# Kernel optimization log

Measured on AMD Instinct MI355X. Metric: run time of the kernel, lower is better.

## Reference

```python
import jax, jax.numpy as jnp
import numpy as np

T, B, V = 512, 64, 1296
S = 30            # fixed target length per sample (targets are concatenated B*S)
BLANK = 0
NEG = -1e30       # -inf surrogate, safe under logaddexp


def setup_inputs() -> dict:
    key = jax.random.key(0)
    k1, k2, k3 = jax.random.split(key, 3)
    logits = jax.random.normal(k1, (T, B, V), dtype=jnp.float32)
    log_probs = jax.nn.log_softmax(logits, axis=-1)  # valid log-prob input to CTC
    # targets are gloss ids in [1, V) (blank=0 excluded), concatenated layout
    targets = jax.random.randint(k2, (B * S,), 1, V, dtype=jnp.int64)
    input_lengths = jax.random.randint(k3, (B,), T // 2, T + 1, dtype=jnp.int32)
    target_lengths = jnp.full((B,), S, dtype=jnp.int32)
    return {"log_probs": log_probs, "targets": targets,
            "input_lengths": input_lengths, "target_lengths": target_lengths}


def _ctc_loss(log_probs, targets2d, input_lengths, target_lengths):
    # log_probs: (T,B,V); targets2d: (B,S)
    L = 2 * S + 1
    b_idx = jnp.arange(B)
    # extended label sequence with interleaved blanks: (B, L)
    ext = jnp.zeros((B, L), dtype=targets2d.dtype).at[:, 1::2].set(targets2d)
    # emission log-probs on lattice positions: lp[t,b,l] = log_probs[t,b,ext[b,l]]
    lp = jnp.take_along_axis(log_probs,
                             jnp.broadcast_to(ext[None, :, :], (T, B, L)), axis=2)
    # skip transition allowed where ext[l] != blank and ext[l] != ext[l-2]
    ext_m2 = jnp.pad(ext[:, :-2], ((0, 0), (2, 0)), constant_values=BLANK)
    allow = (ext != BLANK) & (ext != ext_m2)  # (B, L)

    alpha0 = jnp.full((B, L), NEG, dtype=log_probs.dtype)
    alpha0 = alpha0.at[:, 0].set(lp[0, :, 0]).at[:, 1].set(lp[0, :, 1])

    def step(alpha, lp_t):
        prev1 = jnp.pad(alpha[:, :-1], ((0, 0), (1, 0)), constant_values=NEG)
        prev2 = jnp.pad(alpha[:, :-2], ((0, 0), (2, 0)), constant_values=NEG)
        m = jnp.logaddexp(alpha, prev1)
        m = jnp.where(allow, jnp.logaddexp(m, prev2), m)
        new = m + lp_t
        return new, new

    _, alphas = jax.lax.scan(step, alpha0, lp[1:])          # (T-1, B, L)
    alphas = jnp.concatenate([alpha0[None], alphas], axis=0)  # (T, B, L)

    # alpha at each sample's final frame
    alpha_T = alphas[input_lengths - 1, b_idx]               # (B, L)
    tl = target_lengths.astype(jnp.int32)
    a_last_blank = alpha_T[b_idx, 2 * tl]
    a_last_label = alpha_T[b_idx, 2 * tl - 1]
    loss = -jnp.logaddexp(a_last_blank, a_last_label)        # (B,)
    # zero_infinity=True: infeasible alignments contribute 0
    loss = jnp.where(loss >= 1e29, 0.0, loss)
    # reduction='mean': per-sample loss / target_length, then batch mean
    return jnp.mean(loss / target_lengths.astype(loss.dtype))


def reference(log_probs, targets, input_lengths, target_lengths):
    targets2d = targets.reshape(B, S)  # all target_lengths == S (concatenated layout)
    return _ctc_loss(log_probs, targets2d, input_lengths, target_lengths)
```

## Files before the change

### kernel.cpp

```cpp
#include <hip/hip_runtime.h>

#define T_DIM 512
#define B_DIM 64
#define V_DIM 1296
#define S_DIM 30
#define LN2   0.6931471805599453f

template<int CTRL, bool BC>
__device__ __forceinline__ float dppf(float src, float old) {
    return __int_as_float(__builtin_amdgcn_update_dpp(
        __float_as_int(old), __float_as_int(src), CTRL, 0xF, 0xF, BC));
}

struct ScanSt { float p0, p1; int E; };

template<int MODE>
__device__ __forceinline__ void consume_chunk(const float2* __restrict__ ringc,
                                              int c, int len, int jl, bool is16,
                                              float skipw, int l, ScanSt& st)
{
    float p0 = st.p0, p1 = st.p1;
    int   E  = st.E;
    float2 buf[8];
#pragma unroll
    for (int i = 0; i < 8; ++i) buf[i] = ringc[i * 32 + jl];
#pragma unroll
    for (int i = 0; i < 32; ++i) {
        float2 w = buf[i & 7];
        if (i + 8 < 32) buf[i & 7] = ringc[(i + 8) * 32 + jl];
        if (MODE == 0 && i == 0) {
            p0 = (l == 0) ? ldexpf(w.x, 64) : 0.f;
            p1 = (l == 0) ? ldexpf(w.y, 64) : 0.f;
            E = 64;
        } else {
            float shr = dppf<0x111, true >(p1, 0.f);
            float bcv = dppf<0x142, false>(p1, p1);
            float p1m = is16 ? bcv : shr;
            float np1 = fmaf(skipw, p1m, p0 + p1) * w.y;
            float np0 = (p0 + p1m) * w.x;
            if (MODE == 2) {
                bool act = (c * 32 + i) < len;
                p0 = act ? np0 : p0;
                p1 = act ? np1 : p1;
            } else {
                p0 = np0; p1 = np1;
            }
        }
        if ((i & 7) == 7) {
            float m = fmaxf(p0, p1);
            m = fmaxf(m, dppf<0x111, true >(m, 0.f));
            m = fmaxf(m, dppf<0x112, true >(m, 0.f));
            m = fmaxf(m, dppf<0x114, true >(m, 0.f));
            m = fmaxf(m, dppf<0x118, true >(m, 0.f));
            m = fmaxf(m, dppf<0x142, false>(m, m));
            int eb  = (__float_as_int(m) >> 23) & 0xFF;
            int e31 = __builtin_amdgcn_readlane(eb, 31);
            int s   = 191 - e31;
            p0 = ldexpf(p0, s);
            p1 = ldexpf(p1, s);
            E += s;
        }
    }
    st.p0 = p0; st.p1 = p1; st.E = E;
}

__device__ __forceinline__ void stage_chunk(int k, int b, int trow, int lab, int p,
                                            const float* __restrict__ lp,
                                            float2* __restrict__ ring)
{
    int t0 = k * 32 + trow;
    const float* r0 = lp + ((size_t)t0 * B_DIM + b) * V_DIM;
    const float* r1 = r0 + (size_t)16 * B_DIM * V_DIM;
    float b0 = r0[0], l0 = r0[lab];
    float b1 = r1[0], l1 = r1[lab];
    float2* slot = ring + (size_t)(k & 3) * 1024;
    slot[p]       = make_float2(__expf(b0), __expf(l0));
    slot[p + 512] = make_float2(__expf(b1), __expf(l1));
}

__global__ __launch_bounds__(576)
void ctc_fused_kernel(const float* __restrict__ log_probs,
                      const int*   __restrict__ targets,
                      const int*   __restrict__ input_lengths,
                      const int*   __restrict__ target_lengths,
                      float*       __restrict__ loss_ws)
{
    __shared__ float2 ring[4 * 1024];
    const int  b    = blockIdx.x;
    const int  tid  = threadIdx.x;
    const int  len  = input_lengths[b];
    const bool prod = (tid < 512);

    const int j    = tid & 31;
    const int trow = (tid & 511) >> 5;
    int lab = 0;
    const int l  = tid - 512;
    const int jl = tid & 31;
    ScanSt st = {0.f, 0.f, 0};
    float skipw = 0.f;
    bool  is16  = false;

    if (prod) {
        lab = (j < S_DIM) ? targets[b * S_DIM + j] : 0;
        stage_chunk(0, b, trow, lab, tid, log_probs, ring);
        stage_chunk(1, b, trow, lab, tid, log_probs, ring);
        stage_chunk(2, b, trow, lab, tid, log_probs, ring);
    } else {
        is16 = (l == 16);
        bool allow = (l == 0);
        if (l >= 1 && l < S_DIM)
            allow = (targets[b * S_DIM + l] != targets[b * S_DIM + l - 1]);
        skipw = allow ? 1.f : 0.f;
    }
    __syncthreads();

    for (int c = 0; c < 16; ++c) {
        if (prod) {
            if (c < 13) stage_chunk(c + 3, b, trow, lab, tid, log_probs, ring);
        } else {
            const float2* ringc = ring + (size_t)(c & 3) * 1024;
            if (c == 0)                   consume_chunk<0>(ringc, c, len, jl, is16, skipw, l, st);
            else if ((c + 1) * 32 <= len) consume_chunk<1>(ringc, c, len, jl, is16, skipw, l, st);
            else if (c * 32 < len)        consume_chunk<2>(ringc, c, len, jl, is16, skipw, l, st);
        }
        __syncthreads();
    }

    if (!prod) {
        float pB = __shfl(st.p0, 30);
        float pL = __shfl(st.p1, 29);
        if (l == 0) {
            int   tl   = target_lengths[b];
            float sum  = pB + pL;
            float loss = -LN2 * (__builtin_amdgcn_logf(sum) - (float)st.E);
            if (!(loss < 1e29f)) loss = 0.f;
            loss_ws[b] = loss / (float)tl;
        }
    }
}

__global__ __launch_bounds__(64)
void ctc_reduce_kernel(const float* __restrict__ loss_ws, float* __restrict__ out)
{
    float v = loss_ws[threadIdx.x];
#pragma unroll
    for (int off = 32; off >= 1; off >>= 1)
        v += __shfl_xor(v, off);
    if (threadIdx.x == 0) out[0] = v / (float)B_DIM;
}

extern "C" void kernel_launch(void* const* d_in, const int* in_sizes, int n_in,
                              void* d_out, int out_size, void* d_ws, size_t ws_size,
                              hipStream_t stream)
{
    const float* log_probs      = (const float*)d_in[0];
    const int*   targets        = (const int*)  d_in[1];
    const int*   input_lengths  = (const int*)  d_in[2];
    const int*   target_lengths = (const int*)  d_in[3];
    float*       out            = (float*)d_out;
    float*       losses         = (float*)d_ws;

    hipLaunchKernelGGL(ctc_fused_kernel, dim3(B_DIM), dim3(576), 0, stream,
                       log_probs, targets, input_lengths, target_lengths, losses);
    hipLaunchKernelGGL(ctc_reduce_kernel, dim3(1), dim3(64), 0, stream, losses, out);
}
```

Measured before the change: 32.37 us.

## Pack four lattice states per lane, prefetch rows into registers, fuse final reduction

The scan wave now holds four lattice states per lane as packed float2 vectors, so the 61-state lattice fits in 16 lanes and the max reduction needs fewer DPP steps. Those reduction steps are spread across iterations so they overlap with the recurrence. Producers prefetch log-prob rows into registers two chunks ahead and write float4 ring entries, which hides global latency behind the barriers. The separate reduce kernel is replaced by an atomic counter with a last-block reduction, which adds a memset and a global atomic in exchange for one fewer kernel launch.

```diff
diff --git a/kernel.cpp b/kernel.cpp
--- a/kernel.cpp
+++ b/kernel.cpp
@@ -6,76 +6,87 @@
 #define S_DIM 30
 #define LN2   0.6931471805599453f
 
+typedef float v2f __attribute__((ext_vector_type(2)));
+
 template<int CTRL, bool BC>
 __device__ __forceinline__ float dppf(float src, float old) {
     return __int_as_float(__builtin_amdgcn_update_dpp(
         __float_as_int(old), __float_as_int(src), CTRL, 0xF, 0xF, BC));
 }
 
-struct ScanSt { float p0, p1; int E; };
-
 template<int MODE>
-__device__ __forceinline__ void consume_chunk(const float2* __restrict__ ringc,
-                                              int c, int len, int jl, bool is16,
-                                              float skipw, int l, ScanSt& st)
-{
-    float p0 = st.p0, p1 = st.p1;
-    int   E  = st.E;
-    float2 buf[8];
+__device__ __forceinline__ void consume_chunk(const float4* __restrict__ ringc,
+                                              int c, int len, int lane, v2f S,
+                                              v2f& X, v2f& Y, int& E)
+{
+    const int jl = lane & 15;
+    float4 buf[8];
 #pragma unroll
-    for (int i = 0; i < 8; ++i) buf[i] = ringc[i * 32 + jl];
+    for (int i = 0; i < 8; ++i) buf[i] = ringc[i * 16 + jl];
+
+    float mred = 0.f;
 #pragma unroll
     for (int i = 0; i < 32; ++i) {
-        float2 w = buf[i & 7];
-        if (i + 8 < 32) buf[i & 7] = ringc[(i + 8) * 32 + jl];
+        float4 w = buf[i & 7];
+        if (i + 8 < 32) buf[i & 7] = ringc[(i + 8) * 16 + jl];
+
         if (MODE == 0 && i == 0) {
-            p0 = (l == 0) ? ldexpf(w.x, 64) : 0.f;
-            p1 = (l == 0) ? ldexpf(w.y, 64) : 0.f;
+            bool l0 = (lane == 0);
+            X = (v2f){ l0 ? ldexpf(w.z, 64) : 0.f, 0.f };
+            Y = (v2f){ l0 ? ldexpf(w.x, 64) : 0.f, 0.f };
             E = 64;
         } else {
-            float shr = dppf<0x111, true >(p1, 0.f);
-            float bcv = dppf<0x142, false>(p1, p1);
-            float p1m = is16 ? bcv : shr;
-            float np1 = fmaf(skipw, p1m, p0 + p1) * w.y;
-            float np0 = (p0 + p1m) * w.x;
+            float q3m = dppf<0x111, true>(Y.y, 0.f);
+            v2f Z  = { q3m, Y.x };
+            v2f T1 = X + Z;
+            v2f T2 = X + Y;
+            v2f T3 = __builtin_elementwise_fma(S, Z, T2);
+            v2f Wb = { w.z, w.w };
+            v2f Wl = { w.x, w.y };
+            v2f Xn = T1 * Wb;
+            v2f Yn = T3 * Wl;
             if (MODE == 2) {
                 bool act = (c * 32 + i) < len;
-                p0 = act ? np0 : p0;
-                p1 = act ? np1 : p1;
-            } else {
-                p0 = np0; p1 = np1;
-            }
-        }
+                X = act ? Xn : X;
+                Y = act ? Yn : Y;
+            } else { X = Xn; Y = Yn; }
+        }
+
+        if ((i & 7) == 3) mred = fmaxf(fmaxf(X.x, X.y), fmaxf(Y.x, Y.y));
+        if ((i & 7) == 4) mred = fmaxf(mred, dppf<0x111, true>(mred, 0.f));
+        if ((i & 7) == 5) mred = fmaxf(mred, dppf<0x112, true>(mred, 0.f));
+        if ((i & 7) == 6) mred = fmaxf(mred, dppf<0x114, true>(mred, 0.f));
         if ((i & 7) == 7) {
-            float m = fmaxf(p0, p1);
-            m = fmaxf(m, dppf<0x111, true >(m, 0.f));
-            m = fmaxf(m, dppf<0x112, true >(m, 0.f));
-            m = fmaxf(m, dppf<0x114, true >(m, 0.f));
-            m = fmaxf(m, dppf<0x118, true >(m, 0.f));
-            m = fmaxf(m, dppf<0x142, false>(m, m));
-            int eb  = (__float_as_int(m) >> 23) & 0xFF;
-            int e31 = __builtin_amdgcn_readlane(eb, 31);
-            int s   = 191 - e31;
-            p0 = ldexpf(p0, s);
-            p1 = ldexpf(p1, s);
+            mred = fmaxf(mred, dppf<0x118, true>(mred, 0.f));
+            int e15 = (__builtin_amdgcn_readlane(__float_as_int(mred), 15) >> 23) & 0xFF;
+            int s = 191 - e15;
+            X = (v2f){ ldexpf(X.x, s), ldexpf(X.y, s) };
+            Y = (v2f){ ldexpf(Y.x, s), ldexpf(Y.y, s) };
             E += s;
         }
     }
-    st.p0 = p0; st.p1 = p1; st.E = E;
-}
-
-__device__ __forceinline__ void stage_chunk(int k, int b, int trow, int lab, int p,
-                                            const float* __restrict__ lp,
-                                            float2* __restrict__ ring)
-{
-    int t0 = k * 32 + trow;
-    const float* r0 = lp + ((size_t)t0 * B_DIM + b) * V_DIM;
-    const float* r1 = r0 + (size_t)16 * B_DIM * V_DIM;
-    float b0 = r0[0], l0 = r0[lab];
-    float b1 = r1[0], l1 = r1[lab];
-    float2* slot = ring + (size_t)(k & 3) * 1024;
-    slot[p]       = make_float2(__expf(b0), __expf(l0));
-    slot[p + 512] = make_float2(__expf(b1), __expf(l1));
+}
+
+struct PReg { float a, b, c; };
+
+__device__ __forceinline__ PReg load_rows(const float* __restrict__ lpb,
+                                          int k, int r, int lab0, int lab1)
+{
+    const float* row = lpb + (size_t)(k * 32 + r) * (B_DIM * V_DIM);
+    PReg x;
+    x.a = row[lab0];
+    x.b = row[lab1];
+    x.c = row[0];
+    return x;
+}
+
+__device__ __forceinline__ void write_chunk(float4* __restrict__ ring, int k, int p,
+                                            int q, const PReg& x)
+{
+    float wz = __expf(x.c);
+    float wx = (q < 15) ? __expf(x.a) : 0.f;
+    float wy = (q < 15) ? __expf(x.b) : 0.f;
+    ring[(size_t)(k & 3) * 512 + p] = make_float4(wx, wy, wz, wz);
 }
 
 __global__ __launch_bounds__(576)
@@ -83,70 +94,91 @@
                       const int*   __restrict__ targets,
                       const int*   __restrict__ input_lengths,
                       const int*   __restrict__ target_lengths,
-                      float*       __restrict__ loss_ws)
-{
-    __shared__ float2 ring[4 * 1024];
+                      float*       __restrict__ losses,
+                      unsigned*    __restrict__ counter,
+                      float*       __restrict__ out)
+{
+    __shared__ float4 ring[4 * 512];
     const int  b    = blockIdx.x;
     const int  tid  = threadIdx.x;
     const int  len  = input_lengths[b];
     const bool prod = (tid < 512);
 
-    const int j    = tid & 31;
-    const int trow = (tid & 511) >> 5;
-    int lab = 0;
-    const int l  = tid - 512;
-    const int jl = tid & 31;
-    ScanSt st = {0.f, 0.f, 0};
-    float skipw = 0.f;
-    bool  is16  = false;
+    const int q = tid & 15;
+    const int r = (tid & 511) >> 4;
+    int lab0 = 0, lab1 = 0;
+    PReg rA = {0,0,0}, rB = {0,0,0};
+    const float* lpb = log_probs + (size_t)b * V_DIM;
+
+    const int lane = tid - 512;
+    v2f X = {0.f, 0.f}, Y = {0.f, 0.f}, S = {0.f, 0.f};
+    int E = 0;
 
     if (prod) {
-        lab = (j < S_DIM) ? targets[b * S_DIM + j] : 0;
-        stage_chunk(0, b, trow, lab, tid, log_probs, ring);
-        stage_chunk(1, b, trow, lab, tid, log_probs, ring);
-        stage_chunk(2, b, trow, lab, tid, log_probs, ring);
+        int i0 = b * S_DIM + ((2 * q     < S_DIM) ? 2 * q     : 0);
+        int i1 = b * S_DIM + ((2 * q + 1 < S_DIM) ? 2 * q + 1 : 0);
+        lab0 = targets[i0];
+        lab1 = targets[i1];
+        PReg t0 = load_rows(lpb, 0, r, lab0, lab1);
+        PReg t1 = load_rows(lpb, 1, r, lab0, lab1);
+        PReg t2 = load_rows(lpb, 2, r, lab0, lab1);
+        rA = load_rows(lpb, 3, r, lab0, lab1);
+        rB = load_rows(lpb, 4, r, lab0, lab1);
+        write_chunk(ring, 0, tid, q, t0);
+        write_chunk(ring, 1, tid, q, t1);
+        write_chunk(ring, 2, tid, q, t2);
     } else {
-        is16 = (l == 16);
-        bool allow = (l == 0);
-        if (l >= 1 && l < S_DIM)
-            allow = (targets[b * S_DIM + l] != targets[b * S_DIM + l - 1]);
-        skipw = allow ? 1.f : 0.f;
+        int lq = lane & 15;
+        float s0 = 0.f, s1 = 0.f;
+        if (lq < 15) {
+            int k0 = 2 * lq;
+            int tc = targets[b * S_DIM + k0];
+            int tp = (k0 > 0) ? targets[b * S_DIM + k0 - 1] : -1;
+            s0 = (tc != tp) ? 1.f : 0.f;
+            int tn = targets[b * S_DIM + k0 + 1];
+            s1 = (tn != tc) ? 1.f : 0.f;
+        }
+        S = (v2f){ s0, s1 };
     }
     __syncthreads();
 
     for (int c = 0; c < 16; ++c) {
         if (prod) {
-            if (c < 13) stage_chunk(c + 3, b, trow, lab, tid, log_probs, ring);
+            if (c < 13) write_chunk(ring, c + 3, tid, q, rA);
+            PReg nl = {0,0,0};
+            if (c < 11) nl = load_rows(lpb, c + 5, r, lab0, lab1);
+            rA = rB; rB = nl;
         } else {
-            const float2* ringc = ring + (size_t)(c & 3) * 1024;
-            if (c == 0)                   consume_chunk<0>(ringc, c, len, jl, is16, skipw, l, st);
-            else if ((c + 1) * 32 <= len) consume_chunk<1>(ringc, c, len, jl, is16, skipw, l, st);
-            else if (c * 32 < len)        consume_chunk<2>(ringc, c, len, jl, is16, skipw, l, st);
+            const float4* ringc = &ring[(size_t)(c & 3) * 512];
+            if (c == 0)                   consume_chunk<0>(ringc, c, len, lane, S, X, Y, E);
+            else if ((c + 1) * 32 <= len) consume_chunk<1>(ringc, c, len, lane, S, X, Y, E);
+            else if (c * 32 < len)        consume_chunk<2>(ringc, c, len, lane, S, X, Y, E);
         }
         __syncthreads();
     }
 
     if (!prod) {
-        float pB = __shfl(st.p0, 30);
-        float pL = __shfl(st.p1, 29);
-        if (l == 0) {
-            int   tl   = target_lengths[b];
-            float sum  = pB + pL;
-            float loss = -LN2 * (__builtin_amdgcn_logf(sum) - (float)st.E);
+        int tl   = target_lengths[b];
+        int pB_p = 2 * tl, pL_p = 2 * tl - 1;
+        float vB = (pB_p & 2) ? ((pB_p & 1) ? Y.y : X.y) : ((pB_p & 1) ? Y.x : X.x);
+        float vL = (pL_p & 2) ? ((pL_p & 1) ? Y.y : X.y) : ((pL_p & 1) ? Y.x : X.x);
+        float pB = __shfl(vB, pB_p >> 2);
+        float pL = __shfl(vL, pL_p >> 2);
+        if (lane == 0) {
+            float loss = -LN2 * (__builtin_amdgcn_logf(pB + pL) - (float)E);
             if (!(loss < 1e29f)) loss = 0.f;
-            loss_ws[b] = loss / (float)tl;
-        }
-    }
-}
-
-__global__ __launch_bounds__(64)
-void ctc_reduce_kernel(const float* __restrict__ loss_ws, float* __restrict__ out)
-{
-    float v = loss_ws[threadIdx.x];
-#pragma unroll
-    for (int off = 32; off >= 1; off >>= 1)
-        v += __shfl_xor(v, off);
-    if (threadIdx.x == 0) out[0] = v / (float)B_DIM;
+            losses[b] = loss / (float)tl;
+            __threadfence();
+            unsigned old = atomicAdd(counter, 1u);
+            if (old == 63u) {
+                __threadfence();
+                float sum = 0.f;
+                for (int i = 0; i < B_DIM; ++i)
+                    sum += ((volatile const float*)losses)[i];
+                out[0] = sum * (1.f / (float)B_DIM);
+            }
+        }
+    }
 }
 
 extern "C" void kernel_launch(void* const* d_in, const int* in_sizes, int n_in,
@@ -159,8 +191,10 @@
     const int*   target_lengths = (const int*)  d_in[3];
     float*       out            = (float*)d_out;
     float*       losses         = (float*)d_ws;
-
+    unsigned*    counter        = (unsigned*)((char*)d_ws + 256);
+
+    hipMemsetAsync(counter, 0, sizeof(unsigned), stream);
     hipLaunchKernelGGL(ctc_fused_kernel, dim3(B_DIM), dim3(576), 0, stream,
-                       log_probs, targets, input_lengths, target_lengths, losses);
-    hipLaunchKernelGGL(ctc_reduce_kernel, dim3(1), dim3(64), 0, stream, losses, out);
-}
+                       log_probs, targets, input_lengths, target_lengths,
+                       losses, counter, out);
+}
```

Measured after the change: 40.22 us. 1.24x slower.
